# Kernel tuning notes

Hardware: AMD Instinct MI355X
Metric: run time of the kernel (lower is better)

The kernel has to match this reference:

```python
import jax, jax.numpy as jnp
import numpy as np

C_IN, C_OUT = 64, 32
SD, RFF = 2, 16
RF = 0.05          # receptive_field percentile
TEMP = 1.0
EPS = 1e-8
RFF_STD = 6.0


def setup_inputs() -> dict:
    key = jax.random.key(0)
    ks = jax.random.split(key, 10)
    B_, T, V, Q = 2, 4, 2048, 512
    x = jax.random.normal(ks[0], (B_, T, V, C_IN), dtype=jnp.float32)
    pos = jax.random.uniform(ks[1], (V, SD), dtype=jnp.float32)
    query_pos = jax.random.uniform(ks[2], (Q, SD), dtype=jnp.float32)
    s = 1.0 / np.sqrt(C_IN)
    W_lin = jax.random.uniform(ks[3], (C_IN, C_IN), minval=-s, maxval=s, dtype=jnp.float32)
    b_lin = jax.random.uniform(ks[4], (C_IN,), minval=-s, maxval=s, dtype=jnp.float32)
    Bmat = RFF_STD * jax.random.normal(ks[5], (SD, RFF), dtype=jnp.float32)
    s1 = 1.0 / np.sqrt(32)
    W1 = jax.random.uniform(ks[6], (32, 32), minval=-s1, maxval=s1, dtype=jnp.float32)
    b1 = jax.random.uniform(ks[7], (32,), minval=-s1, maxval=s1, dtype=jnp.float32)
    W2 = jax.random.uniform(ks[8], (C_IN * C_OUT, 32), minval=-s1, maxval=s1, dtype=jnp.float32)
    sf = np.sqrt(3.0 / C_IN)
    filt = jax.random.uniform(ks[9], (C_IN * C_OUT,), minval=-sf, maxval=sf, dtype=jnp.float32)
    bias = jnp.zeros((C_OUT,), dtype=jnp.float32)
    return {"x": x, "pos": pos, "query_pos": query_pos, "W_lin": W_lin, "b_lin": b_lin,
            "Bmat": Bmat, "W1": W1, "b1": b1, "W2": W2, "filt": filt, "bias": bias}


def reference(x, pos, query_pos, W_lin, b_lin, Bmat, W1, b1, W2, filt, bias):
    # pairwise periodic displacement / squared distance
    dist = query_pos[:, None, :] - pos[None, :, :]            # (Q, V, 2)
    dist = (dist + 0.5) % 1.0 - 0.5                           # periodic wrap
    edist = jnp.sum(dist ** 2, axis=-1)                       # (Q, V)
    # quantile threshold -> max neighbourhood size (eager, data-dependent like torch)
    thr = jnp.quantile(edist, RF, axis=-1, keepdims=True)     # linear interpolation, as torch
    K = int(jnp.max(jnp.sum(edist <= thr, axis=-1)))
    _, ind = jax.lax.top_k(-edist, K)                         # (Q, K) nearest neighbours
    # gather per-query neighbour displacements / distances
    d_g = jnp.take_along_axis(dist, ind[..., None], axis=1)   # (Q, K, 2)
    e_g = jnp.take_along_axis(edist, ind, axis=1)[..., None]  # (Q, K, 1)
    e_g = e_g - jnp.min(e_g, axis=-2, keepdims=True)
    e_g = e_g / (jnp.max(e_g, axis=-2, keepdims=True) + EPS)
    k_dist = jax.nn.softmax(-e_g / TEMP, axis=-2)             # (Q, K, 1)
    # random Fourier features + kernel MLP
    proj = 2.0 * jnp.pi * (d_g @ Bmat)                        # (Q, K, 16)
    kfeat = jnp.concatenate([jnp.sin(proj), jnp.cos(proj)], axis=-1)  # (Q, K, 32)
    h = jax.nn.gelu(kfeat @ W1.T + b1, approximate=False)
    ker = (h @ W2.T + filt) * k_dist                          # (Q, K, C_IN*C_OUT)
    ker = ker.reshape(ker.shape[0], ker.shape[1], C_IN, C_OUT)
    # point-wise linear on features, then gather + contract
    xl = x @ W_lin.T + b_lin                                  # (B, T, V, C_IN)
    xg = xl[:, :, ind, :]                                     # (B, T, Q, K, C_IN)
    return jnp.einsum('qvcd,btqvc->btqd', ker, xg) + bias     # (B, T, Q, C_OUT)
```

## Files before the change

kernel.cpp:

```cpp
#include <hip/hip_runtime.h>

#define K_SEL 103
typedef unsigned long long ull_t;
typedef _Float16 f16x8 __attribute__((ext_vector_type(8)));
typedef float f32x4 __attribute__((ext_vector_type(4)));

__global__ __launch_bounds__(512, 6) void k12(const float* __restrict__ pos,
                                              const float* __restrict__ qpos,
                                              const float* __restrict__ Bmat,
                                              const float* __restrict__ W1,
                                              const float* __restrict__ b1,
                                              _Float16* __restrict__ Hh,
                                              int* __restrict__ indg,
                                              float* __restrict__ invtot,
                                              const float* __restrict__ x,
                                              const float* __restrict__ W,
                                              const float* __restrict__ b,
                                              _Float16* __restrict__ xlh,
                                              const float* __restrict__ W2,
                                              const float* __restrict__ filt,
                                              _Float16* __restrict__ W2th) {
    __shared__ __align__(16) unsigned char smem[30880];
    const int tid = threadIdx.x;
    const int bid = blockIdx.x;
    const int lane = tid & 63;
    const int wid = tid >> 6;

    if (bid >= 512) {
        const int bb = bid - 512;
        float* Wt = (float*)smem;
        if (tid < 264) {
            int t = bb * 264 + tid;
            int d = t & 31;
            int e = t >> 5;
            int c = e & 63;
            int j = e >> 6;
            float v = (j < 32) ? W2[(c * 32 + d) * 32 + j] : filt[c * 32 + d];
            W2th[d * 2112 + e] = (_Float16)v;
        }
        for (int t = tid; t < 4096; t += 512)
            Wt[(t & 63) * 65 + (t >> 6)] = W[t];
        __syncthreads();
        const int i = tid & 63;
        const int sub = tid >> 6;
        const float bi = b[i];
        #pragma unroll
        for (int rr = 0; rr < 2; ++rr) {
            const int r0 = bb * 64 + rr * 32 + sub * 4;
            float acc0 = bi, acc1 = bi, acc2 = bi, acc3 = bi;
            const float* xr = x + (size_t)r0 * 64;
            #pragma unroll 4
            for (int jj = 0; jj < 16; ++jj) {
                float4 v0 = *(const float4*)(xr + 0 * 64 + jj * 4);
                float4 v1 = *(const float4*)(xr + 1 * 64 + jj * 4);
                float4 v2 = *(const float4*)(xr + 2 * 64 + jj * 4);
                float4 v3 = *(const float4*)(xr + 3 * 64 + jj * 4);
                float w0 = Wt[(jj * 4 + 0) * 65 + i];
                float w1 = Wt[(jj * 4 + 1) * 65 + i];
                float w2 = Wt[(jj * 4 + 2) * 65 + i];
                float w3 = Wt[(jj * 4 + 3) * 65 + i];
                acc0 += v0.x * w0 + v0.y * w1 + v0.z * w2 + v0.w * w3;
                acc1 += v1.x * w0 + v1.y * w1 + v1.z * w2 + v1.w * w3;
                acc2 += v2.x * w0 + v2.y * w1 + v2.z * w2 + v2.w * w3;
                acc3 += v3.x * w0 + v3.y * w1 + v3.z * w2 + v3.w * w3;
            }
            xlh[(size_t)(r0 + 0) * 64 + i] = (_Float16)acc0;
            xlh[(size_t)(r0 + 1) * 64 + i] = (_Float16)acc1;
            xlh[(size_t)(r0 + 2) * 64 + i] = (_Float16)acc2;
            xlh[(size_t)(r0 + 3) * 64 + i] = (_Float16)acc3;
        }
        return;
    }

    const int q = bid;
    unsigned* ebits   = (unsigned*)(smem);
    unsigned* hist    = (unsigned*)(smem + 8192);
    _Float16* Hs      = (_Float16*)(smem + 8192);
    float*    W1s     = (float*)(smem + 24576);
    float*    b1s     = (float*)(smem + 28672);
    float*    Bm      = (float*)(smem + 28800);
    int*      sel_v   = (int*)(smem + 28928);
    float*    sel_e   = (float*)(smem + 29344);
    ull_t*    bnd     = (ull_t*)(smem + 29760);
    int*      counters= (int*)(smem + 30784);
    int*      info    = (int*)(smem + 30792);
    float*    wred    = (float*)(smem + 30800);
    float*    emax_s  = (float*)(smem + 30832);
    unsigned* wscan   = (unsigned*)(smem + 30836);

    for (int t = tid; t < 1024; t += 512) W1s[t] = W1[t];
    if (tid < 32) { b1s[tid] = b1[tid]; Bm[tid] = Bmat[tid]; }
    if (tid < 2)  counters[tid] = 0;
    for (int t = tid; t < 1024; t += 512) ((uint4*)hist)[t] = make_uint4(0, 0, 0, 0);
    const float qp0 = qpos[q * 2 + 0];
    const float qp1 = qpos[q * 2 + 1];
    __syncthreads();

    float lmin = 1e30f;
    for (int v = tid; v < 2048; v += 512) {
        float2 p = ((const float2*)pos)[v];
        float d0 = qp0 - p.x;
        float d1 = qp1 - p.y;
        d0 += 0.5f; d0 -= floorf(d0); d0 -= 0.5f;
        d1 += 0.5f; d1 -= floorf(d1); d1 -= 0.5f;
        float e = d0 * d0 + d1 * d1;
        ebits[v] = __float_as_uint(e);
        lmin = fminf(lmin, e);
        int bb2 = (int)(e * 8192.0f); bb2 = (bb2 > 4095) ? 4095 : bb2;
        atomicAdd(&hist[bb2], 1u);
    }
    #pragma unroll
    for (int off = 32; off > 0; off >>= 1)
        lmin = fminf(lmin, __shfl_xor(lmin, off, 64));
    if (lane == 0) wred[wid] = lmin;
    __syncthreads();
    float e_min = wred[0];
    #pragma unroll
    for (int w2 = 1; w2 < 8; ++w2) e_min = fminf(e_min, wred[w2]);

    unsigned lsum = 0;
    #pragma unroll
    for (int i = 0; i < 8; ++i) lsum += hist[tid * 8 + i];
    unsigned vq = lsum;
    #pragma unroll
    for (int off = 1; off < 64; off <<= 1) {
        unsigned n = __shfl_up(vq, off, 64);
        if (lane >= off) vq += n;
    }
    if (lane == 63) wscan[wid] = vq;
    __syncthreads();
    unsigned base = 0;
    for (int w2 = 0; w2 < wid; ++w2) base += wscan[w2];
    unsigned cum = base + vq - lsum;
    #pragma unroll
    for (int i = 0; i < 8; ++i) {
        unsigned cnt = hist[tid * 8 + i];
        if (cum <= 102u && 102u < cum + cnt) { info[0] = tid * 8 + i; info[1] = (int)cum; }
        cum += cnt;
    }
    __syncthreads();
    const int Bstar = info[0];
    const int L = info[1];
    const int need = K_SEL - L;

    {
        f16x8 z = {0, 0, 0, 0, 0, 0, 0, 0};
        for (int t = tid; t < 768; t += 512) ((f16x8*)Hs)[t] = z;
    }
    for (int v = tid; v < 2048; v += 512) {
        unsigned bb2 = ebits[v];
        float e = __uint_as_float(bb2);
        int bin = (int)(e * 8192.0f); bin = (bin > 4095) ? 4095 : bin;
        if (bin < Bstar) {
            int s2 = atomicAdd(&counters[0], 1);
            sel_v[s2] = v; sel_e[s2] = e;
        } else if (bin == Bstar) {
            int s2 = atomicAdd(&counters[1], 1);
            if (s2 < 128) bnd[s2] = (((ull_t)bb2) << 32) | (unsigned)v;
        }
    }
    __syncthreads();
    {
        int nb = counters[1]; if (nb > 128) nb = 128;
        if (tid < nb) {
            ull_t my = bnd[tid];
            int rank = 0;
            for (int i = 0; i < nb; ++i) rank += (bnd[i] < my);
            if (rank < need) {
                sel_v[L + rank] = (int)(unsigned)(my & 0xffffffffull);
                sel_e[L + rank] = __uint_as_float((unsigned)(my >> 32));
            }
            if (rank == need - 1)
                emax_s[0] = __uint_as_float((unsigned)(my >> 32));
        }
    }
    __syncthreads();

    const float denom = (emax_s[0] - e_min) + 1e-8f;
    float w = 0.0f;
    if (tid < K_SEL) {
        w = __expf(-(sel_e[tid] - e_min) / denom);
        sel_e[tid] = w;
    }
    float sw = w;
    #pragma unroll
    for (int off = 32; off > 0; off >>= 1)
        sw += __shfl_xor(sw, off, 64);
    if (lane == 0) wred[wid] = sw;
    __syncthreads();
    if (tid == 0) {
        float tot = 0.0f;
        #pragma unroll
        for (int w2 = 0; w2 < 8; ++w2) tot += wred[w2];
        invtot[q] = 1.0f / tot;
    }

    if (tid < 4 * K_SEL) {
        const int k = tid >> 2;
        const int io = (tid & 3) * 8;
        const int v = sel_v[k];
        const float wk = sel_e[k];
        float2 p = ((const float2*)pos)[v];
        float d0 = qp0 - p.x;
        float d1 = qp1 - p.y;
        d0 += 0.5f; d0 -= floorf(d0); d0 -= 0.5f;
        d1 += 0.5f; d1 -= floorf(d1); d1 -= 0.5f;
        float kf[32];
        #pragma unroll
        for (int f = 0; f < 16; ++f) {
            float t = d0 * Bm[f] + d1 * Bm[16 + f];
            float r = t - rintf(t);
            kf[f]      = __builtin_amdgcn_sinf(r);
            kf[16 + f] = __builtin_amdgcn_cosf(r);
        }
        #pragma unroll
        for (int i = io; i < io + 8; ++i) {
            float pre = b1s[i];
            #pragma unroll
            for (int jf = 0; jf < 32; ++jf) pre += kf[jf] * W1s[i * 32 + jf];
            float g = 0.5f * pre * (1.0f + erff(pre * 0.70710678118654752f));
            Hs[i * 128 + k] = (_Float16)(g * wk);
        }
        if (io == 0) {
            Hs[32 * 128 + k] = (_Float16)wk;
            indg[q * K_SEL + k] = v;
        }
    }
    __syncthreads();
    {
        _Float16* hq = Hh + (size_t)q * 6144;
        for (int t = tid; t < 768; t += 512)
            ((f16x8*)hq)[t] = ((const f16x8*)Hs)[t];
    }
}

__global__ __launch_bounds__(512, 4) void k3_main(const _Float16* __restrict__ xlh,
                                                  const _Float16* __restrict__ Hh,
                                                  const int* __restrict__ indg,
                                                  const _Float16* __restrict__ W2th,
                                                  const float* __restrict__ bias,
                                                  const float* __restrict__ invtot,
                                                  float* __restrict__ out) {
    const int q = blockIdx.x;
    const int tid = threadIdx.x;
    const int lane = tid & 63;
    const int wid = tid >> 6;
    const int h   = wid >> 2;
    const int cq  = wid & 3;
    const int n0 = lane & 15;
    const int quad = lane >> 4;

    __shared__ __align__(16) unsigned char smem[69376];
    _Float16* Xg  = (_Float16*)smem;
    _Float16* Zh8 = (_Float16*)(smem + 35072);
    int* ind_s    = (int*)(smem + 68864);
    float* red    = (float*)smem;

    const _Float16* hq = Hh + (size_t)q * 6144;
    f16x8 afr[4][3];
    #pragma unroll
    for (int ks = 0; ks < 4; ++ks)
        #pragma unroll
        for (int r = 0; r < 3; ++r)
            afr[ks][r] = *(const f16x8*)(hq + (r * 16 + n0) * 128 + ks * 32 + quad * 8);
    const float it = invtot[q];
    const int e0f = wid * 32 + quad * 8;
    f16x8 pf0 = *(const f16x8*)(W2th + (size_t)(0 * 16 + n0) * 2112 + e0f);
    f16x8 pf1 = *(const f16x8*)(W2th + (size_t)(1 * 16 + n0) * 2112 + e0f);
    if (tid < 128) {
        int kk = (tid < K_SEL) ? tid : tid - K_SEL;
        ind_s[tid] = indg[q * K_SEL + kk];
    }
    __syncthreads();

    int g_k[4], g_oct[4], g_h[4];
    #pragma unroll
    for (int i = 0; i < 4; ++i) {
        int t = tid + i * 512;
        g_h[i] = t >> 10;
        g_k[i] = (t >> 3) & 127;
        g_oct[i] = t & 7;
    }

    {
        f16x8 v0[4];
        #pragma unroll
        for (int i = 0; i < 4; ++i)
            v0[i] = *(const f16x8*)(xlh + ((size_t)g_h[i] * 2048 + ind_s[g_k[i]]) * 64 + g_oct[i] * 8);
        #pragma unroll
        for (int i = 0; i < 4; ++i) {
            int base = g_h[i] * 8768 + g_oct[i] * 1096 + g_k[i];
            #pragma unroll
            for (int jj = 0; jj < 8; ++jj) Xg[base + 136 * jj] = v0[i][jj];
        }
    }
    __syncthreads();

    const int cA = cq * 16 + n0;
    const int cswz = h * 8768 + cA * 136 + ((cA >> 3) << 3);

    #pragma unroll
    for (int p = 0; p < 4; ++p) {
        f16x8 vn[4];
        if (p < 3) {
            #pragma unroll
            for (int i = 0; i < 4; ++i)
                vn[i] = *(const f16x8*)(xlh + ((size_t)(2 * (p + 1) + g_h[i]) * 2048 + ind_s[g_k[i]]) * 64 + g_oct[i] * 8);
        }
        f32x4 Dz[3];
        #pragma unroll
        for (int r = 0; r < 3; ++r) Dz[r] = (f32x4){0.f, 0.f, 0.f, 0.f};
        #pragma unroll
        for (int ks = 0; ks < 4; ++ks) {
            f16x8 bfr = *(const f16x8*)(&Xg[cswz + ks * 32 + quad * 8]);
            #pragma unroll
            for (int r = 0; r < 3; ++r)
                Dz[r] = __builtin_amdgcn_mfma_f32_16x16x32_f16(afr[ks][r], bfr, Dz[r], 0, 0, 0);
        }
        __syncthreads();
        const int bt = 2 * p + h;
        #pragma unroll
        for (int r = 0; r < 3; ++r)
            #pragma unroll
            for (int reg = 0; reg < 4; ++reg) {
                int j = r * 16 + quad * 4 + reg;
                if (j < 33) Zh8[bt * 2112 + j * 64 + cA] = (_Float16)Dz[r][reg];
            }
        if (p < 3) {
            #pragma unroll
            for (int i = 0; i < 4; ++i) {
                int base = g_h[i] * 8768 + g_oct[i] * 1096 + g_k[i];
                #pragma unroll
                for (int jj = 0; jj < 8; ++jj) Xg[base + 136 * jj] = vn[i][jj];
            }
            __syncthreads();
        }
    }
    __syncthreads();

    f32x4 D2[2][2];
    #pragma unroll
    for (int pp = 0; pp < 2; ++pp)
        #pragma unroll
        for (int dt = 0; dt < 2; ++dt) D2[pp][dt] = (f32x4){0.f, 0.f, 0.f, 0.f};
    {
        f16x8 a2 = {0, 0, 0, 0, 0, 0, 0, 0};
        if (n0 < 8) a2 = *(const f16x8*)(&Zh8[n0 * 2112 + e0f]);
        D2[0][0] = __builtin_amdgcn_mfma_f32_16x16x32_f16(a2, pf0, D2[0][0], 0, 0, 0);
        D2[0][1] = __builtin_amdgcn_mfma_f32_16x16x32_f16(a2, pf1, D2[0][1], 0, 0, 0);
    }
    int pp = 1;
    #pragma unroll 2
    for (int s = wid + 8; s < 66; s += 8) {
        const int e0 = s * 32 + quad * 8;
        f16x8 a2 = {0, 0, 0, 0, 0, 0, 0, 0};
        if (n0 < 8) a2 = *(const f16x8*)(&Zh8[n0 * 2112 + e0]);
        #pragma unroll
        for (int dt = 0; dt < 2; ++dt) {
            f16x8 bfr = *(const f16x8*)(W2th + (size_t)(dt * 16 + n0) * 2112 + e0);
            D2[pp][dt] = __builtin_amdgcn_mfma_f32_16x16x32_f16(a2, bfr, D2[pp][dt], 0, 0, 0);
        }
        pp ^= 1;
    }
    #pragma unroll
    for (int dt = 0; dt < 2; ++dt)
        D2[0][dt] = D2[0][dt] + D2[1][dt];

    if (quad < 2) {
        #pragma unroll
        for (int dt = 0; dt < 2; ++dt)
            #pragma unroll
            for (int reg = 0; reg < 4; ++reg)
                red[((wid * 2 + dt) * 8 + quad * 4 + reg) * 16 + n0] = D2[0][dt][reg];
    }
    __syncthreads();
    if (tid < 256) {
        const int bt = tid >> 5;
        const int d = tid & 31;
        const int dt = d >> 4;
        const int dn = d & 15;
        float s = 0.0f;
        #pragma unroll
        for (int w2 = 0; w2 < 8; ++w2)
            s += red[((w2 * 2 + dt) * 8 + bt) * 16 + dn];
        out[((size_t)bt * 512 + q) * 32 + d] = bias[d] + it * s;
    }
}

extern "C" void kernel_launch(void* const* d_in, const int* in_sizes, int n_in,
                              void* d_out, int out_size, void* d_ws, size_t ws_size,
                              hipStream_t stream) {
    const float* x     = (const float*)d_in[0];
    const float* pos   = (const float*)d_in[1];
    const float* qpos  = (const float*)d_in[2];
    const float* W_lin = (const float*)d_in[3];
    const float* b_lin = (const float*)d_in[4];
    const float* Bmat  = (const float*)d_in[5];
    const float* W1    = (const float*)d_in[6];
    const float* b1    = (const float*)d_in[7];
    const float* W2    = (const float*)d_in[8];
    const float* filt  = (const float*)d_in[9];
    const float* bias  = (const float*)d_in[10];
    float* out = (float*)d_out;

    float* ws = (float*)d_ws;
    _Float16* xlh    = (_Float16*)ws;
    _Float16* Hh     = (_Float16*)(ws + 524288);
    int*      indg   = (int*)(ws + 2097152);
    _Float16* W2th   = (_Float16*)(ws + 2150144);
    float*    invtot = ws + 2183936;

    k12<<<768, 512, 0, stream>>>(pos, qpos, Bmat, W1, b1, Hh, indg, invtot,
                                 x, W_lin, b_lin, xlh, W2, filt, W2th);
    k3_main<<<512, 512, 0, stream>>>(xlh, Hh, indg, W2th, bias, invtot, out);
}
```

Before: 113.2 us.

## Fuse neighbour selection and kernel MLP into main contraction kernel

Moves the per-query distance, histogram top-K selection and RFF/GELU hidden computation out of the first kernel and into the main contraction kernel. H, the neighbour indices and the normalisation factor now stay in shared memory instead of round-tripping through global workspace. The first kernel now only does the linear projection and the W2 transpose, launched on 256 blocks. In exchange, the main kernel grows to about 80KB of shared memory with launch bounds lowered to 4 blocks per SM. The selection work also no longer overlaps with the linear-projection blocks.

```diff
diff --git a/kernel.cpp b/kernel.cpp
--- a/kernel.cpp
+++ b/kernel.cpp
@@ -5,385 +5,369 @@
 typedef _Float16 f16x8 __attribute__((ext_vector_type(8)));
 typedef float f32x4 __attribute__((ext_vector_type(4)));
 
-__global__ __launch_bounds__(512, 6) void k12(const float* __restrict__ pos,
-                                              const float* __restrict__ qpos,
-                                              const float* __restrict__ Bmat,
-                                              const float* __restrict__ W1,
-                                              const float* __restrict__ b1,
-                                              _Float16* __restrict__ Hh,
-                                              int* __restrict__ indg,
-                                              float* __restrict__ invtot,
-                                              const float* __restrict__ x,
-                                              const float* __restrict__ W,
-                                              const float* __restrict__ b,
-                                              _Float16* __restrict__ xlh,
-                                              const float* __restrict__ W2,
-                                              const float* __restrict__ filt,
-                                              _Float16* __restrict__ W2th) {
-    __shared__ __align__(16) unsigned char smem[30880];
+__global__ __launch_bounds__(512, 6) void klin(const float* __restrict__ x,
+                                               const float* __restrict__ W,
+                                               const float* __restrict__ b,
+                                               _Float16* __restrict__ xlh,
+                                               const float* __restrict__ W2,
+                                               const float* __restrict__ filt,
+                                               _Float16* __restrict__ W2th) {
+    __shared__ __align__(16) float Wt[64 * 65];
     const int tid = threadIdx.x;
-    const int bid = blockIdx.x;
+    const int bb = blockIdx.x;
+    if (tid < 264) {
+        int t = bb * 264 + tid;
+        int d = t & 31;
+        int e = t >> 5;
+        int c = e & 63;
+        int j = e >> 6;
+        float v = (j < 32) ? W2[(c * 32 + d) * 32 + j] : filt[c * 32 + d];
+        W2th[d * 2112 + e] = (_Float16)v;
+    }
+    for (int t = tid; t < 4096; t += 512)
+        Wt[(t & 63) * 65 + (t >> 6)] = W[t];
+    __syncthreads();
+    const int i = tid & 63;
+    const int sub = tid >> 6;
+    const float bi = b[i];
+    #pragma unroll
+    for (int rr = 0; rr < 2; ++rr) {
+        const int r0 = bb * 64 + rr * 32 + sub * 4;
+        float acc0 = bi, acc1 = bi, acc2 = bi, acc3 = bi;
+        const float* xr = x + (size_t)r0 * 64;
+        #pragma unroll 4
+        for (int jj = 0; jj < 16; ++jj) {
+            float4 v0 = *(const float4*)(xr + 0 * 64 + jj * 4);
+            float4 v1 = *(const float4*)(xr + 1 * 64 + jj * 4);
+            float4 v2 = *(const float4*)(xr + 2 * 64 + jj * 4);
+            float4 v3 = *(const float4*)(xr + 3 * 64 + jj * 4);
+            float w0 = Wt[(jj * 4 + 0) * 65 + i];
+            float w1 = Wt[(jj * 4 + 1) * 65 + i];
+            float w2 = Wt[(jj * 4 + 2) * 65 + i];
+            float w3 = Wt[(jj * 4 + 3) * 65 + i];
+            acc0 += v0.x * w0 + v0.y * w1 + v0.z * w2 + v0.w * w3;
+            acc1 += v1.x * w0 + v1.y * w1 + v1.z * w2 + v1.w * w3;
+            acc2 += v2.x * w0 + v2.y * w1 + v2.z * w2 + v2.w * w3;
+            acc3 += v3.x * w0 + v3.y * w1 + v3.z * w2 + v3.w * w3;
+        }
+        xlh[(size_t)(r0 + 0) * 64 + i] = (_Float16)acc0;
+        xlh[(size_t)(r0 + 1) * 64 + i] = (_Float16)acc1;
+        xlh[(size_t)(r0 + 2) * 64 + i] = (_Float16)acc2;
+        xlh[(size_t)(r0 + 3) * 64 + i] = (_Float16)acc3;
+    }
+}
+
+__global__ __launch_bounds__(512, 4) void kmain(const float* __restrict__ pos,
+                                                const float* __restrict__ qpos,
+                                                const float* __restrict__ Bmat,
+                                                const float* __restrict__ W1,
+                                                const float* __restrict__ b1,
+                                                const _Float16* __restrict__ xlh,
+                                                const _Float16* __restrict__ W2th,
+                                                const float* __restrict__ bias,
+                                                float* __restrict__ out) {
+    __shared__ __align__(16) unsigned char smem[81680];
+    _Float16* Hs    = (_Float16*)smem;
+    int*      ind   = (int*)(smem + 12288);
+    float*    inv_s = (float*)(smem + 12800);
+    unsigned char* SG = smem + 12816;
+
+    const int tid = threadIdx.x;
+    const int q = blockIdx.x;
     const int lane = tid & 63;
     const int wid = tid >> 6;
 
-    if (bid >= 512) {
-        const int bb = bid - 512;
-        float* Wt = (float*)smem;
-        if (tid < 264) {
-            int t = bb * 264 + tid;
-            int d = t & 31;
-            int e = t >> 5;
-            int c = e & 63;
-            int j = e >> 6;
-            float v = (j < 32) ? W2[(c * 32 + d) * 32 + j] : filt[c * 32 + d];
-            W2th[d * 2112 + e] = (_Float16)v;
-        }
-        for (int t = tid; t < 4096; t += 512)
-            Wt[(t & 63) * 65 + (t >> 6)] = W[t];
-        __syncthreads();
-        const int i = tid & 63;
-        const int sub = tid >> 6;
-        const float bi = b[i];
-        #pragma unroll
-        for (int rr = 0; rr < 2; ++rr) {
-            const int r0 = bb * 64 + rr * 32 + sub * 4;
-            float acc0 = bi, acc1 = bi, acc2 = bi, acc3 = bi;
-            const float* xr = x + (size_t)r0 * 64;
-            #pragma unroll 4
-            for (int jj = 0; jj < 16; ++jj) {
-                float4 v0 = *(const float4*)(xr + 0 * 64 + jj * 4);
-                float4 v1 = *(const float4*)(xr + 1 * 64 + jj * 4);
-                float4 v2 = *(const float4*)(xr + 2 * 64 + jj * 4);
-                float4 v3 = *(const float4*)(xr + 3 * 64 + jj * 4);
-                float w0 = Wt[(jj * 4 + 0) * 65 + i];
-                float w1 = Wt[(jj * 4 + 1) * 65 + i];
-                float w2 = Wt[(jj * 4 + 2) * 65 + i];
-                float w3 = Wt[(jj * 4 + 3) * 65 + i];
-                acc0 += v0.x * w0 + v0.y * w1 + v0.z * w2 + v0.w * w3;
-                acc1 += v1.x * w0 + v1.y * w1 + v1.z * w2 + v1.w * w3;
-                acc2 += v2.x * w0 + v2.y * w1 + v2.z * w2 + v2.w * w3;
-                acc3 += v3.x * w0 + v3.y * w1 + v3.z * w2 + v3.w * w3;
-            }
-            xlh[(size_t)(r0 + 0) * 64 + i] = (_Float16)acc0;
-            xlh[(size_t)(r0 + 1) * 64 + i] = (_Float16)acc1;
-            xlh[(size_t)(r0 + 2) * 64 + i] = (_Float16)acc2;
-            xlh[(size_t)(r0 + 3) * 64 + i] = (_Float16)acc3;
-        }
-        return;
+    {
+        unsigned* ebits   = (unsigned*)(SG);
+        unsigned* hist    = (unsigned*)(SG + 8192);
+        float*    W1s     = (float*)(SG + 24576);
+        float*    b1s     = (float*)(SG + 28672);
+        float*    Bm      = (float*)(SG + 28800);
+        int*      sel_v   = (int*)(SG + 28928);
+        float*    sel_e   = (float*)(SG + 29344);
+        ull_t*    bnd     = (ull_t*)(SG + 29760);
+        int*      counters= (int*)(SG + 30784);
+        int*      info    = (int*)(SG + 30792);
+        float*    wred    = (float*)(SG + 30800);
+        float*    emax_s  = (float*)(SG + 30832);
+        unsigned* wscan   = (unsigned*)(SG + 30836);
+
+        for (int t = tid; t < 1024; t += 512) W1s[t] = W1[t];
+        if (tid < 32) { b1s[tid] = b1[tid]; Bm[tid] = Bmat[tid]; }
+        if (tid < 2)  counters[tid] = 0;
+        for (int t = tid; t < 1024; t += 512) ((uint4*)hist)[t] = make_uint4(0, 0, 0, 0);
+        const float qp0 = qpos[q * 2 + 0];
+        const float qp1 = qpos[q * 2 + 1];
+        __syncthreads();
+
+        float lmin = 1e30f;
+        for (int v = tid; v < 2048; v += 512) {
+            float2 p = ((const float2*)pos)[v];
+            float d0 = qp0 - p.x;
+            float d1 = qp1 - p.y;
+            d0 += 0.5f; d0 -= floorf(d0); d0 -= 0.5f;
+            d1 += 0.5f; d1 -= floorf(d1); d1 -= 0.5f;
+            float e = d0 * d0 + d1 * d1;
+            ebits[v] = __float_as_uint(e);
+            lmin = fminf(lmin, e);
+            int bb2 = (int)(e * 8192.0f); bb2 = (bb2 > 4095) ? 4095 : bb2;
+            atomicAdd(&hist[bb2], 1u);
+        }
+        #pragma unroll
+        for (int off = 32; off > 0; off >>= 1)
+            lmin = fminf(lmin, __shfl_xor(lmin, off, 64));
+        if (lane == 0) wred[wid] = lmin;
+        __syncthreads();
+        float e_min = wred[0];
+        #pragma unroll
+        for (int w2 = 1; w2 < 8; ++w2) e_min = fminf(e_min, wred[w2]);
+
+        unsigned lsum = 0;
+        #pragma unroll
+        for (int i = 0; i < 8; ++i) lsum += hist[tid * 8 + i];
+        unsigned vq = lsum;
+        #pragma unroll
+        for (int off = 1; off < 64; off <<= 1) {
+            unsigned n = __shfl_up(vq, off, 64);
+            if (lane >= off) vq += n;
+        }
+        if (lane == 63) wscan[wid] = vq;
+        __syncthreads();
+        unsigned base = 0;
+        for (int w2 = 0; w2 < wid; ++w2) base += wscan[w2];
+        unsigned cum = base + vq - lsum;
+        #pragma unroll
+        for (int i = 0; i < 8; ++i) {
+            unsigned cnt = hist[tid * 8 + i];
+            if (cum <= 102u && 102u < cum + cnt) { info[0] = tid * 8 + i; info[1] = (int)cum; }
+            cum += cnt;
+        }
+        __syncthreads();
+        const int Bstar = info[0];
+        const int L = info[1];
+        const int need = K_SEL - L;
+
+        {
+            f16x8 z = {0, 0, 0, 0, 0, 0, 0, 0};
+            for (int t = tid; t < 768; t += 512) ((f16x8*)Hs)[t] = z;
+        }
+        for (int v = tid; v < 2048; v += 512) {
+            unsigned bb2 = ebits[v];
+            float e = __uint_as_float(bb2);
+            int bin = (int)(e * 8192.0f); bin = (bin > 4095) ? 4095 : bin;
+            if (bin < Bstar) {
+                int s2 = atomicAdd(&counters[0], 1);
+                sel_v[s2] = v; sel_e[s2] = e;
+            } else if (bin == Bstar) {
+                int s2 = atomicAdd(&counters[1], 1);
+                if (s2 < 128) bnd[s2] = (((ull_t)bb2) << 32) | (unsigned)v;
+            }
+        }
+        __syncthreads();
+        {
+            int nb = counters[1]; if (nb > 128) nb = 128;
+            if (tid < nb) {
+                ull_t my = bnd[tid];
+                int rank = 0;
+                for (int i = 0; i < nb; ++i) rank += (bnd[i] < my);
+                if (rank < need) {
+                    sel_v[L + rank] = (int)(unsigned)(my & 0xffffffffull);
+                    sel_e[L + rank] = __uint_as_float((unsigned)(my >> 32));
+                }
+                if (rank == need - 1)
+                    emax_s[0] = __uint_as_float((unsigned)(my >> 32));
+            }
+        }
+        __syncthreads();
+
+        const float denom = (emax_s[0] - e_min) + 1e-8f;
+        float w = 0.0f;
+        if (tid < K_SEL) {
+            w = __expf(-(sel_e[tid] - e_min) / denom);
+            sel_e[tid] = w;
+        }
+        float sw = w;
+        #pragma unroll
+        for (int off = 32; off > 0; off >>= 1)
+            sw += __shfl_xor(sw, off, 64);
+        if (lane == 0) wred[wid] = sw;
+        __syncthreads();
+        if (tid == 0) {
+            float tot = 0.0f;
+            #pragma unroll
+            for (int w2 = 0; w2 < 8; ++w2) tot += wred[w2];
+            inv_s[0] = 1.0f / tot;
+        }
+
+        if (tid < 4 * K_SEL) {
+            const int k = tid >> 2;
+            const int io = (tid & 3) * 8;
+            const int v = sel_v[k];
+            const float wk = sel_e[k];
+            float2 p = ((const float2*)pos)[v];
+            float d0 = qp0 - p.x;
+            float d1 = qp1 - p.y;
+            d0 += 0.5f; d0 -= floorf(d0); d0 -= 0.5f;
+            d1 += 0.5f; d1 -= floorf(d1); d1 -= 0.5f;
+            float kf[32];
+            #pragma unroll
+            for (int f = 0; f < 16; ++f) {
+                float t = d0 * Bm[f] + d1 * Bm[16 + f];
+                float r = t - rintf(t);
+                kf[f]      = __builtin_amdgcn_sinf(r);
+                kf[16 + f] = __builtin_amdgcn_cosf(r);
+            }
+            #pragma unroll
+            for (int i = io; i < io + 8; ++i) {
+                float pre = b1s[i];
+                #pragma unroll
+                for (int jf = 0; jf < 32; ++jf) pre += kf[jf] * W1s[i * 32 + jf];
+                float g = 0.5f * pre * (1.0f + erff(pre * 0.70710678118654752f));
+                Hs[i * 128 + k] = (_Float16)(g * wk);
+            }
+            if (io == 0) {
+                Hs[32 * 128 + k] = (_Float16)wk;
+                ind[k] = v;
+            }
+        }
+        __syncthreads();
+        if (tid < 128 - K_SEL) ind[K_SEL + tid] = ind[tid];
     }
 
-    const int q = bid;
-    unsigned* ebits   = (unsigned*)(smem);
-    unsigned* hist    = (unsigned*)(smem + 8192);
-    _Float16* Hs      = (_Float16*)(smem + 8192);
-    float*    W1s     = (float*)(smem + 24576);
-    float*    b1s     = (float*)(smem + 28672);
-    float*    Bm      = (float*)(smem + 28800);
-    int*      sel_v   = (int*)(smem + 28928);
-    float*    sel_e   = (float*)(smem + 29344);
-    ull_t*    bnd     = (ull_t*)(smem + 29760);
-    int*      counters= (int*)(smem + 30784);
-    int*      info    = (int*)(smem + 30792);
-    float*    wred    = (float*)(smem + 30800);
-    float*    emax_s  = (float*)(smem + 30832);
-    unsigned* wscan   = (unsigned*)(smem + 30836);
-
-    for (int t = tid; t < 1024; t += 512) W1s[t] = W1[t];
-    if (tid < 32) { b1s[tid] = b1[tid]; Bm[tid] = Bmat[tid]; }
-    if (tid < 2)  counters[tid] = 0;
-    for (int t = tid; t < 1024; t += 512) ((uint4*)hist)[t] = make_uint4(0, 0, 0, 0);
-    const float qp0 = qpos[q * 2 + 0];
-    const float qp1 = qpos[q * 2 + 1];
-    __syncthreads();
-
-    float lmin = 1e30f;
-    for (int v = tid; v < 2048; v += 512) {
-        float2 p = ((const float2*)pos)[v];
-        float d0 = qp0 - p.x;
-        float d1 = qp1 - p.y;
-        d0 += 0.5f; d0 -= floorf(d0); d0 -= 0.5f;
-        d1 += 0.5f; d1 -= floorf(d1); d1 -= 0.5f;
-        float e = d0 * d0 + d1 * d1;
-        ebits[v] = __float_as_uint(e);
-        lmin = fminf(lmin, e);
-        int bb2 = (int)(e * 8192.0f); bb2 = (bb2 > 4095) ? 4095 : bb2;
-        atomicAdd(&hist[bb2], 1u);
-    }
-    #pragma unroll
-    for (int off = 32; off > 0; off >>= 1)
-        lmin = fminf(lmin, __shfl_xor(lmin, off, 64));
-    if (lane == 0) wred[wid] = lmin;
-    __syncthreads();
-    float e_min = wred[0];
-    #pragma unroll
-    for (int w2 = 1; w2 < 8; ++w2) e_min = fminf(e_min, wred[w2]);
-
-    unsigned lsum = 0;
-    #pragma unroll
-    for (int i = 0; i < 8; ++i) lsum += hist[tid * 8 + i];
-    unsigned vq = lsum;
-    #pragma unroll
-    for (int off = 1; off < 64; off <<= 1) {
-        unsigned n = __shfl_up(vq, off, 64);
-        if (lane >= off) vq += n;
-    }
-    if (lane == 63) wscan[wid] = vq;
-    __syncthreads();
-    unsigned base = 0;
-    for (int w2 = 0; w2 < wid; ++w2) base += wscan[w2];
-    unsigned cum = base + vq - lsum;
-    #pragma unroll
-    for (int i = 0; i < 8; ++i) {
-        unsigned cnt = hist[tid * 8 + i];
-        if (cum <= 102u && 102u < cum + cnt) { info[0] = tid * 8 + i; info[1] = (int)cum; }
-        cum += cnt;
-    }
-    __syncthreads();
-    const int Bstar = info[0];
-    const int L = info[1];
-    const int need = K_SEL - L;
-
     {
-        f16x8 z = {0, 0, 0, 0, 0, 0, 0, 0};
-        for (int t = tid; t < 768; t += 512) ((f16x8*)Hs)[t] = z;
-    }
-    for (int v = tid; v < 2048; v += 512) {
-        unsigned bb2 = ebits[v];
-        float e = __uint_as_float(bb2);
-        int bin = (int)(e * 8192.0f); bin = (bin > 4095) ? 4095 : bin;
-        if (bin < Bstar) {
-            int s2 = atomicAdd(&counters[0], 1);
-            sel_v[s2] = v; sel_e[s2] = e;
-        } else if (bin == Bstar) {
-            int s2 = atomicAdd(&counters[1], 1);
-            if (s2 < 128) bnd[s2] = (((ull_t)bb2) << 32) | (unsigned)v;
-        }
-    }
-    __syncthreads();
-    {
-        int nb = counters[1]; if (nb > 128) nb = 128;
-        if (tid < nb) {
-            ull_t my = bnd[tid];
-            int rank = 0;
-            for (int i = 0; i < nb; ++i) rank += (bnd[i] < my);
-            if (rank < need) {
-                sel_v[L + rank] = (int)(unsigned)(my & 0xffffffffull);
-                sel_e[L + rank] = __uint_as_float((unsigned)(my >> 32));
-            }
-            if (rank == need - 1)
-                emax_s[0] = __uint_as_float((unsigned)(my >> 32));
-        }
-    }
-    __syncthreads();
-
-    const float denom = (emax_s[0] - e_min) + 1e-8f;
-    float w = 0.0f;
-    if (tid < K_SEL) {
-        w = __expf(-(sel_e[tid] - e_min) / denom);
-        sel_e[tid] = w;
-    }
-    float sw = w;
-    #pragma unroll
-    for (int off = 32; off > 0; off >>= 1)
-        sw += __shfl_xor(sw, off, 64);
-    if (lane == 0) wred[wid] = sw;
-    __syncthreads();
-    if (tid == 0) {
-        float tot = 0.0f;
-        #pragma unroll
-        for (int w2 = 0; w2 < 8; ++w2) tot += wred[w2];
-        invtot[q] = 1.0f / tot;
-    }
-
-    if (tid < 4 * K_SEL) {
-        const int k = tid >> 2;
-        const int io = (tid & 3) * 8;
-        const int v = sel_v[k];
-        const float wk = sel_e[k];
-        float2 p = ((const float2*)pos)[v];
-        float d0 = qp0 - p.x;
-        float d1 = qp1 - p.y;
-        d0 += 0.5f; d0 -= floorf(d0); d0 -= 0.5f;
-        d1 += 0.5f; d1 -= floorf(d1); d1 -= 0.5f;
-        float kf[32];
-        #pragma unroll
-        for (int f = 0; f < 16; ++f) {
-            float t = d0 * Bm[f] + d1 * Bm[16 + f];
-            float r = t - rintf(t);
-            kf[f]      = __builtin_amdgcn_sinf(r);
-            kf[16 + f] = __builtin_amdgcn_cosf(r);
-        }
-        #pragma unroll
-        for (int i = io; i < io + 8; ++i) {
-            float pre = b1s[i];
-            #pragma unroll
-            for (int jf = 0; jf < 32; ++jf) pre += kf[jf] * W1s[i * 32 + jf];
-            float g = 0.5f * pre * (1.0f + erff(pre * 0.70710678118654752f));
-            Hs[i * 128 + k] = (_Float16)(g * wk);
-        }
-        if (io == 0) {
-            Hs[32 * 128 + k] = (_Float16)wk;
-            indg[q * K_SEL + k] = v;
-        }
-    }
-    __syncthreads();
-    {
-        _Float16* hq = Hh + (size_t)q * 6144;
-        for (int t = tid; t < 768; t += 512)
-            ((f16x8*)hq)[t] = ((const f16x8*)Hs)[t];
-    }
-}
-
-__global__ __launch_bounds__(512, 4) void k3_main(const _Float16* __restrict__ xlh,
-                                                  const _Float16* __restrict__ Hh,
-                                                  const int* __restrict__ indg,
-                                                  const _Float16* __restrict__ W2th,
-                                                  const float* __restrict__ bias,
-                                                  const float* __restrict__ invtot,
-                                                  float* __restrict__ out) {
-    const int q = blockIdx.x;
-    const int tid = threadIdx.x;
-    const int lane = tid & 63;
-    const int wid = tid >> 6;
-    const int h   = wid >> 2;
-    const int cq  = wid & 3;
-    const int n0 = lane & 15;
-    const int quad = lane >> 4;
-
-    __shared__ __align__(16) unsigned char smem[69376];
-    _Float16* Xg  = (_Float16*)smem;
-    _Float16* Zh8 = (_Float16*)(smem + 35072);
-    int* ind_s    = (int*)(smem + 68864);
-    float* red    = (float*)smem;
-
-    const _Float16* hq = Hh + (size_t)q * 6144;
-    f16x8 afr[4][3];
-    #pragma unroll
-    for (int ks = 0; ks < 4; ++ks)
-        #pragma unroll
-        for (int r = 0; r < 3; ++r)
-            afr[ks][r] = *(const f16x8*)(hq + (r * 16 + n0) * 128 + ks * 32 + quad * 8);
-    const float it = invtot[q];
-    const int e0f = wid * 32 + quad * 8;
-    f16x8 pf0 = *(const f16x8*)(W2th + (size_t)(0 * 16 + n0) * 2112 + e0f);
-    f16x8 pf1 = *(const f16x8*)(W2th + (size_t)(1 * 16 + n0) * 2112 + e0f);
-    if (tid < 128) {
-        int kk = (tid < K_SEL) ? tid : tid - K_SEL;
-        ind_s[tid] = indg[q * K_SEL + kk];
-    }
-    __syncthreads();
-
-    int g_k[4], g_oct[4], g_h[4];
-    #pragma unroll
-    for (int i = 0; i < 4; ++i) {
-        int t = tid + i * 512;
-        g_h[i] = t >> 10;
-        g_k[i] = (t >> 3) & 127;
-        g_oct[i] = t & 7;
-    }
-
-    {
-        f16x8 v0[4];
-        #pragma unroll
-        for (int i = 0; i < 4; ++i)
-            v0[i] = *(const f16x8*)(xlh + ((size_t)g_h[i] * 2048 + ind_s[g_k[i]]) * 64 + g_oct[i] * 8);
+        const int h   = wid >> 2;
+        const int cq  = wid & 3;
+        const int n0 = lane & 15;
+        const int quad = lane >> 4;
+
+        _Float16* Xg  = (_Float16*)SG;
+        _Float16* Zh8 = (_Float16*)(SG + 35072);
+        float* red    = (float*)SG;
+
+        f16x8 afr[4][3];
+        #pragma unroll
+        for (int ks = 0; ks < 4; ++ks)
+            #pragma unroll
+            for (int r = 0; r < 3; ++r)
+                afr[ks][r] = *(const f16x8*)(Hs + (r * 16 + n0) * 128 + ks * 32 + quad * 8);
+        const float it = inv_s[0];
+        const int e0f = wid * 32 + quad * 8;
+        f16x8 pf0 = *(const f16x8*)(W2th + (size_t)(0 * 16 + n0) * 2112 + e0f);
+        f16x8 pf1 = *(const f16x8*)(W2th + (size_t)(1 * 16 + n0) * 2112 + e0f);
+        __syncthreads();
+
+        int g_k[4], g_oct[4], g_h[4];
         #pragma unroll
         for (int i = 0; i < 4; ++i) {
-            int base = g_h[i] * 8768 + g_oct[i] * 1096 + g_k[i];
-            #pragma unroll
-            for (int jj = 0; jj < 8; ++jj) Xg[base + 136 * jj] = v0[i][jj];
-        }
-    }
-    __syncthreads();
-
-    const int cA = cq * 16 + n0;
-    const int cswz = h * 8768 + cA * 136 + ((cA >> 3) << 3);
-
-    #pragma unroll
-    for (int p = 0; p < 4; ++p) {
-        f16x8 vn[4];
-        if (p < 3) {
+            int t = tid + i * 512;
+            g_h[i] = t >> 10;
+            g_k[i] = (t >> 3) & 127;
+            g_oct[i] = t & 7;
+        }
+
+        {
+            f16x8 v0[4];
             #pragma unroll
             for (int i = 0; i < 4; ++i)
-                vn[i] = *(const f16x8*)(xlh + ((size_t)(2 * (p + 1) + g_h[i]) * 2048 + ind_s[g_k[i]]) * 64 + g_oct[i] * 8);
-        }
-        f32x4 Dz[3];
-        #pragma unroll
-        for (int r = 0; r < 3; ++r) Dz[r] = (f32x4){0.f, 0.f, 0.f, 0.f};
-        #pragma unroll
-        for (int ks = 0; ks < 4; ++ks) {
-            f16x8 bfr = *(const f16x8*)(&Xg[cswz + ks * 32 + quad * 8]);
-            #pragma unroll
-            for (int r = 0; r < 3; ++r)
-                Dz[r] = __builtin_amdgcn_mfma_f32_16x16x32_f16(afr[ks][r], bfr, Dz[r], 0, 0, 0);
-        }
-        __syncthreads();
-        const int bt = 2 * p + h;
-        #pragma unroll
-        for (int r = 0; r < 3; ++r)
-            #pragma unroll
-            for (int reg = 0; reg < 4; ++reg) {
-                int j = r * 16 + quad * 4 + reg;
-                if (j < 33) Zh8[bt * 2112 + j * 64 + cA] = (_Float16)Dz[r][reg];
-            }
-        if (p < 3) {
+                v0[i] = *(const f16x8*)(xlh + ((size_t)g_h[i] * 2048 + ind[g_k[i]]) * 64 + g_oct[i] * 8);
             #pragma unroll
             for (int i = 0; i < 4; ++i) {
                 int base = g_h[i] * 8768 + g_oct[i] * 1096 + g_k[i];
                 #pragma unroll
-                for (int jj = 0; jj < 8; ++jj) Xg[base + 136 * jj] = vn[i][jj];
+                for (int jj = 0; jj < 8; ++jj) Xg[base + 136 * jj] = v0[i][jj];
+            }
+        }
+        __syncthreads();
+
+        const int cA = cq * 16 + n0;
+        const int cswz = h * 8768 + cA * 136 + ((cA >> 3) << 3);
+
+        #pragma unroll
+        for (int p = 0; p < 4; ++p) {
+            f16x8 vn[4];
+            if (p < 3) {
+                #pragma unroll
+                for (int i = 0; i < 4; ++i)
+                    vn[i] = *(const f16x8*)(xlh + ((size_t)(2 * (p + 1) + g_h[i]) * 2048 + ind[g_k[i]]) * 64 + g_oct[i] * 8);
+            }
+            f32x4 Dz[3];
+            #pragma unroll
+            for (int r = 0; r < 3; ++r) Dz[r] = (f32x4){0.f, 0.f, 0.f, 0.f};
+            #pragma unroll
+            for (int ks = 0; ks < 4; ++ks) {
+                f16x8 bfr = *(const f16x8*)(&Xg[cswz + ks * 32 + quad * 8]);
+                #pragma unroll
+                for (int r = 0; r < 3; ++r)
+                    Dz[r] = __builtin_amdgcn_mfma_f32_16x16x32_f16(afr[ks][r], bfr, Dz[r], 0, 0, 0);
             }
             __syncthreads();
-        }
-    }
-    __syncthreads();
-
-    f32x4 D2[2][2];
-    #pragma unroll
-    for (int pp = 0; pp < 2; ++pp)
-        #pragma unroll
-        for (int dt = 0; dt < 2; ++dt) D2[pp][dt] = (f32x4){0.f, 0.f, 0.f, 0.f};
-    {
-        f16x8 a2 = {0, 0, 0, 0, 0, 0, 0, 0};
-        if (n0 < 8) a2 = *(const f16x8*)(&Zh8[n0 * 2112 + e0f]);
-        D2[0][0] = __builtin_amdgcn_mfma_f32_16x16x32_f16(a2, pf0, D2[0][0], 0, 0, 0);
-        D2[0][1] = __builtin_amdgcn_mfma_f32_16x16x32_f16(a2, pf1, D2[0][1], 0, 0, 0);
-    }
-    int pp = 1;
-    #pragma unroll 2
-    for (int s = wid + 8; s < 66; s += 8) {
-        const int e0 = s * 32 + quad * 8;
-        f16x8 a2 = {0, 0, 0, 0, 0, 0, 0, 0};
-        if (n0 < 8) a2 = *(const f16x8*)(&Zh8[n0 * 2112 + e0]);
-        #pragma unroll
-        for (int dt = 0; dt < 2; ++dt) {
-            f16x8 bfr = *(const f16x8*)(W2th + (size_t)(dt * 16 + n0) * 2112 + e0);
-            D2[pp][dt] = __builtin_amdgcn_mfma_f32_16x16x32_f16(a2, bfr, D2[pp][dt], 0, 0, 0);
-        }
-        pp ^= 1;
-    }
-    #pragma unroll
-    for (int dt = 0; dt < 2; ++dt)
-        D2[0][dt] = D2[0][dt] + D2[1][dt];
-
-    if (quad < 2) {
+            const int bt = 2 * p + h;
+            #pragma unroll
+            for (int r = 0; r < 3; ++r)
+                #pragma unroll
+                for (int reg = 0; reg < 4; ++reg) {
+                    int j = r * 16 + quad * 4 + reg;
+                    if (j < 33) Zh8[bt * 2112 + j * 64 + cA] = (_Float16)Dz[r][reg];
+                }
+            if (p < 3) {
+                #pragma unroll
+                for (int i = 0; i < 4; ++i) {
+                    int base = g_h[i] * 8768 + g_oct[i] * 1096 + g_k[i];
+                    #pragma unroll
+                    for (int jj = 0; jj < 8; ++jj) Xg[base + 136 * jj] = vn[i][jj];
+                }
+                __syncthreads();
+            }
+        }
+        __syncthreads();
+
+        f32x4 D2[2][2];
+        #pragma unroll
+        for (int pp = 0; pp < 2; ++pp)
+            #pragma unroll
+            for (int dt = 0; dt < 2; ++dt) D2[pp][dt] = (f32x4){0.f, 0.f, 0.f, 0.f};
+        {
+            f16x8 a2 = {0, 0, 0, 0, 0, 0, 0, 0};
+            if (n0 < 8) a2 = *(const f16x8*)(&Zh8[n0 * 2112 + e0f]);
+            D2[0][0] = __builtin_amdgcn_mfma_f32_16x16x32_f16(a2, pf0, D2[0][0], 0, 0, 0);
+            D2[0][1] = __builtin_amdgcn_mfma_f32_16x16x32_f16(a2, pf1, D2[0][1], 0, 0, 0);
+        }
+        int pp = 1;
+        #pragma unroll 2
+        for (int s = wid + 8; s < 66; s += 8) {
+            const int e0 = s * 32 + quad * 8;
+            f16x8 a2 = {0, 0, 0, 0, 0, 0, 0, 0};
+            if (n0 < 8) a2 = *(const f16x8*)(&Zh8[n0 * 2112 + e0]);
+            #pragma unroll
+            for (int dt = 0; dt < 2; ++dt) {
+                f16x8 bfr = *(const f16x8*)(W2th + (size_t)(dt * 16 + n0) * 2112 + e0);
+                D2[pp][dt] = __builtin_amdgcn_mfma_f32_16x16x32_f16(a2, bfr, D2[pp][dt], 0, 0, 0);
+            }
+            pp ^= 1;
+        }
         #pragma unroll
         for (int dt = 0; dt < 2; ++dt)
-            #pragma unroll
-            for (int reg = 0; reg < 4; ++reg)
-                red[((wid * 2 + dt) * 8 + quad * 4 + reg) * 16 + n0] = D2[0][dt][reg];
-    }
-    __syncthreads();
-    if (tid < 256) {
-        const int bt = tid >> 5;
-        const int d = tid & 31;
-        const int dt = d >> 4;
-        const int dn = d & 15;
-        float s = 0.0f;
-        #pragma unroll
-        for (int w2 = 0; w2 < 8; ++w2)
-            s += red[((w2 * 2 + dt) * 8 + bt) * 16 + dn];
-        out[((size_t)bt * 512 + q) * 32 + d] = bias[d] + it * s;
+            D2[0][dt] = D2[0][dt] + D2[1][dt];
+
+        if (quad < 2) {
+            #pragma unroll
+            for (int dt = 0; dt < 2; ++dt)
+                #pragma unroll
+                for (int reg = 0; reg < 4; ++reg)
+                    red[((wid * 2 + dt) * 8 + quad * 4 + reg) * 16 + n0] = D2[0][dt][reg];
+        }
+        __syncthreads();
+        if (tid < 256) {
+            const int bt = tid >> 5;
+            const int d = tid & 31;
+            const int dt = d >> 4;
+            const int dn = d & 15;
+            float s = 0.0f;
+            #pragma unroll
+            for (int w2 = 0; w2 < 8; ++w2)
+                s += red[((w2 * 2 + dt) * 8 + bt) * 16 + dn];
+            out[((size_t)bt * 512 + q) * 32 + d] = bias[d] + it * s;
+        }
     }
 }
 
@@ -404,13 +388,9 @@
     float* out = (float*)d_out;
 
     float* ws = (float*)d_ws;
-    _Float16* xlh    = (_Float16*)ws;
-    _Float16* Hh     = (_Float16*)(ws + 524288);
-    int*      indg   = (int*)(ws + 2097152);
-    _Float16* W2th   = (_Float16*)(ws + 2150144);
-    float*    invtot = ws + 2183936;
-
-    k12<<<768, 512, 0, stream>>>(pos, qpos, Bmat, W1, b1, Hh, indg, invtot,
-                                 x, W_lin, b_lin, xlh, W2, filt, W2th);
-    k3_main<<<512, 512, 0, stream>>>(xlh, Hh, indg, W2th, bias, invtot, out);
+    _Float16* xlh  = (_Float16*)ws;
+    _Float16* W2th = (_Float16*)(ws + 524288);
+
+    klin<<<256, 512, 0, stream>>>(x, W_lin, b_lin, xlh, W2, filt, W2th);
+    kmain<<<512, 512, 0, stream>>>(pos, qpos, Bmat, W1, b1, xlh, W2th, bias, out);
 }
```

New measurement: 115.7 us. 2.2% more time.
